# Optimization experiments

Hardware: AMD Instinct MI355X
Metric: run time of the kernel (lower is better)

## Reference

```python
import jax, jax.numpy as jnp
import numpy as np

# Crossbar physical constants (SiOx-like, per crossbar.map conventions)
V_REF = 0.25
K_V = 2.0 * V_REF          # k_V = 2 * V_ref
G_OFF = 1e-4
G_ON = 1e-3
EPS = 1e-12


def setup_inputs() -> dict:
    key = jax.random.key(0)
    ks = jax.random.split(key, 4)
    B, n_in, n_out = 128, 1024, 512
    stdv = 1.0 / np.sqrt(n_in)
    x = jax.random.normal(ks[0], (B, n_in), jnp.float32)
    # non-negative double weights, init N(0.5, stdv) clipped to >=0 (NonNeg constraint)
    w_pos = jnp.maximum(0.5 + stdv * jax.random.normal(ks[1], (n_in, n_out), jnp.float32), 0.0)
    w_neg = jnp.maximum(0.5 + stdv * jax.random.normal(ks[2], (n_in, n_out), jnp.float32), 0.0)
    b_pos = 0.5 * jnp.ones((n_out,), jnp.float32)
    b_neg = 0.5 * jnp.ones((n_out,), jnp.float32)
    # per-device I/V nonlinearity parameter n ~ N(2.132, 0.095), one per crossbar device
    n_param = 2.132 + 0.095 * jax.random.normal(ks[3], (n_in + 1, 2 * n_out), jnp.float32)
    return {"x": x, "w_pos": w_pos, "w_neg": w_neg, "b_pos": b_pos,
            "b_neg": b_neg, "n_param": n_param}


def memristor_dense_fwd(x, w_pos, w_neg, b_pos, b_neg, n_param):
    B = x.shape[0]
    # append ones column for bias row of the crossbar
    inputs = jnp.concatenate([x, jnp.ones((B, 1), x.dtype)], axis=1)      # [B, R], R=n_in+1
    cw_pos = jnp.concatenate([w_pos, b_pos[None, :]], axis=0)             # [R, n_out]
    cw_neg = jnp.concatenate([w_neg, b_neg[None, :]], axis=0)             # [R, n_out]
    # interleave pos/neg columns -> [R, 2*n_out]
    combined = jnp.stack([cw_pos, cw_neg], axis=-1).reshape(cw_pos.shape[0], -1)
    # x -> V  (crossbar.map.x_to_V)
    V = K_V * inputs                                                      # [B, R]
    # w -> G  (crossbar.map.double_w_to_G)
    max_w = jnp.max(combined)
    k_G = (G_ON - G_OFF) / max_w
    G = k_G * combined + G_OFF                                            # [R, C], C=2*n_out
    # IVNonlinearity (LinearityNonpreserving): I = G*V_ref*sign(V)*(|V|/V_ref)^log2(n)
    gamma = jnp.log2(n_param)                                             # [R, C]
    log_ratio = jnp.log(jnp.maximum(jnp.abs(V) / V_REF, EPS))             # [B, R]
    I_ind = (G * V_REF)[None, :, :] * jnp.sign(V)[:, :, None] \
        * jnp.exp(log_ratio[:, :, None] * gamma[None, :, :])              # [B, R, C]
    I = jnp.sum(I_ind, axis=1)                                            # [B, C]
    # I -> y  (crossbar.map.I_to_y): pos - neg columns, undo k_V*k_G scaling
    I_total = I[:, 0::2] - I[:, 1::2]                                     # [B, n_out]
    y = I_total / (K_V * k_G)
    return y


def reference(x, w_pos, w_neg, b_pos, b_neg, n_param):
    return memristor_dense_fwd(x, w_pos, w_neg, b_pos, b_neg, n_param)
```

## Files before the change

kernel.cpp:

```cpp
#include <hip/hip_runtime.h>


#define N_IN 1024
#define N_OUT 512
#define NB 128
#define Z 16
#define RPC 32
#define JT 64
#define BT 16

typedef float v2f __attribute__((ext_vector_type(2)));

#define AOFF 1024
#define BOFF (1024 + Z * NB * N_OUT)

__launch_bounds__(256, 4)
__global__ void memristor_mainAB(const float* __restrict__ x,
                                 const float* __restrict__ wp,
                                 const float* __restrict__ wn,
                                 const float* __restrict__ npar,
                                 float* __restrict__ ws) {
    __shared__ float Wg[RPC][4][16][4];
    __shared__ float Lx[RPC][BT][2];

    const int tid = threadIdx.x;
    const int jx = blockIdx.x, by = blockIdx.y, bz = blockIdx.z;
    const int j0 = jx * JT;
    const int b0 = by * BT;

    const int tj4 = tid & 15;
    const int bl  = tid >> 4;

    v2f accA01 = {0.f, 0.f}, accA23 = {0.f, 0.f};
    v2f accB01 = {0.f, 0.f}, accB23 = {0.f, 0.f};
    float m_w = 0.0f;

    for (int c = 0; c < 2; ++c) {
        const int rbase = bz * 64 + c * RPC;
        __syncthreads();
        {
            int rq = tid & 15;
            float2 v = *(const float2*)&x[(b0 + bl) * N_IN + rbase + rq * 2];
            float vv[2] = {v.x, v.y};
            #pragma unroll
            for (int k = 0; k < 2; ++k) {
                float val = vv[k];
                float s = (val > 0.f) ? 1.f : ((val < 0.f) ? -1.f : 0.f);
                float t = fmaxf(2.f * fabsf(val), 1e-12f);
                Lx[rq * 2 + k][bl][0] = __builtin_amdgcn_logf(t);
                Lx[rq * 2 + k][bl][1] = s;
            }
        }
        {
            int rr = tid >> 3;
            int cg = tid & 7;
            int pg0 = (2 * cg) ^ (rr & 15);
            int pg1 = (2 * cg + 1) ^ (rr & 15);
            {
                const float* prow = &wp[(rbase + rr) * N_OUT + j0 + cg * 8];
                const float* nrow = &wn[(rbase + rr) * N_OUT + j0 + cg * 8];
                float4 pa = *(const float4*)&prow[0];
                float4 pb = *(const float4*)&prow[4];
                float4 na = *(const float4*)&nrow[0];
                float4 nb = *(const float4*)&nrow[4];
                *(float4*)&Wg[rr][0][pg0][0] = pa;
                *(float4*)&Wg[rr][0][pg1][0] = pb;
                *(float4*)&Wg[rr][1][pg0][0] = make_float4(pa.x - na.x, pa.y - na.y,
                                                           pa.z - na.z, pa.w - na.w);
                *(float4*)&Wg[rr][1][pg1][0] = make_float4(pb.x - nb.x, pb.y - nb.y,
                                                           pb.z - nb.z, pb.w - nb.w);
                m_w = fmaxf(m_w, fmaxf(fmaxf(pa.x, pa.y), fmaxf(pa.z, pa.w)));
                m_w = fmaxf(m_w, fmaxf(fmaxf(pb.x, pb.y), fmaxf(pb.z, pb.w)));
                m_w = fmaxf(m_w, fmaxf(fmaxf(na.x, na.y), fmaxf(na.z, na.w)));
                m_w = fmaxf(m_w, fmaxf(fmaxf(nb.x, nb.y), fmaxf(nb.z, nb.w)));
            }
            {
                const float* nrow = &npar[(rbase + rr) * (2 * N_OUT) + 2 * j0 + cg * 16];
                float4 f0 = *(const float4*)&nrow[0];
                float4 f1 = *(const float4*)&nrow[4];
                float4 f2 = *(const float4*)&nrow[8];
                float4 f3 = *(const float4*)&nrow[12];
                *(float4*)&Wg[rr][2][pg0][0] = make_float4(
                    __builtin_amdgcn_logf(f0.x), __builtin_amdgcn_logf(f0.z),
                    __builtin_amdgcn_logf(f1.x), __builtin_amdgcn_logf(f1.z));
                *(float4*)&Wg[rr][3][pg0][0] = make_float4(
                    __builtin_amdgcn_logf(f0.y), __builtin_amdgcn_logf(f0.w),
                    __builtin_amdgcn_logf(f1.y), __builtin_amdgcn_logf(f1.w));
                *(float4*)&Wg[rr][2][pg1][0] = make_float4(
                    __builtin_amdgcn_logf(f2.x), __builtin_amdgcn_logf(f2.z),
                    __builtin_amdgcn_logf(f3.x), __builtin_amdgcn_logf(f3.z));
                *(float4*)&Wg[rr][3][pg1][0] = make_float4(
                    __builtin_amdgcn_logf(f2.y), __builtin_amdgcn_logf(f2.w),
                    __builtin_amdgcn_logf(f3.y), __builtin_amdgcn_logf(f3.w));
            }
        }
        __syncthreads();

        #pragma unroll 4
        for (int r = 0; r < RPC; ++r) {
            const float4* wrow = (const float4*)&Wg[r][0][tj4 ^ (r & 15)][0];
            float4 w_p = wrow[0];
            float4 w_d = wrow[16];
            float4 g_p = wrow[32];
            float4 g_n = wrow[48];
            float2 Ls = *(const float2*)&Lx[r][bl][0];
            const float L = Ls.x, s = Ls.y;

            v2f wp01 = {w_p.x, w_p.y}, wp23 = {w_p.z, w_p.w};
            v2f wd01 = {w_d.x, w_d.y}, wd23 = {w_d.z, w_d.w};
            v2f gp01 = {g_p.x, g_p.y}, gp23 = {g_p.z, g_p.w};
            v2f gn01 = {g_n.x, g_n.y}, gn23 = {g_n.z, g_n.w};

            v2f ap01 = L * gp01, ap23 = L * gp23;
            v2f an01 = L * gn01, an23 = L * gn23;
            v2f ep01, ep23, en01, en23;
            ep01.x = __builtin_amdgcn_exp2f(ap01.x); ep01.y = __builtin_amdgcn_exp2f(ap01.y);
            ep23.x = __builtin_amdgcn_exp2f(ap23.x); ep23.y = __builtin_amdgcn_exp2f(ap23.y);
            en01.x = __builtin_amdgcn_exp2f(an01.x); en01.y = __builtin_amdgcn_exp2f(an01.y);
            en23.x = __builtin_amdgcn_exp2f(an23.x); en23.y = __builtin_amdgcn_exp2f(an23.y);

            v2f u01 = ep01 - en01, u23 = ep23 - en23;
            accB01 += s * u01;
            accB23 += s * u23;
            v2f v01 = wp01 * u01 + wd01 * en01;
            v2f v23 = wp23 * u23 + wd23 * en23;
            accA01 += s * v01;
            accA23 += s * v23;
        }
    }

    {
        size_t base = (size_t)bz * (NB * N_OUT) + (b0 + bl) * N_OUT + j0 + tj4 * 4;
        *(float4*)&ws[AOFF + base] = make_float4(accA01.x, accA01.y, accA23.x, accA23.y);
        *(float4*)&ws[BOFF + base] = make_float4(accB01.x, accB01.y, accB23.x, accB23.y);
    }

    if (by == 0) {
        __syncthreads();
        float* qred = &Lx[0][0][0];
        #pragma unroll
        for (int off = 32; off; off >>= 1) m_w = fmaxf(m_w, __shfl_xor(m_w, off));
        if ((tid & 63) == 0) qred[tid >> 6] = m_w;
        __syncthreads();
        if (tid == 0)
            ws[jx * Z + bz] = fmaxf(fmaxf(qred[0], qred[1]), fmaxf(qred[2], qred[3]));
    }
}

__global__ void reduce_combine(const float* __restrict__ ws,
                               const float* __restrict__ bp,
                               const float* __restrict__ bn,
                               const float* __restrict__ npar,
                               float* __restrict__ out) {
    __shared__ float qs[4];
    const int tid = threadIdx.x;

    float mm = (tid < 128) ? ws[tid] : 0.0f;
    float2 a2 = ((const float2*)bp)[tid];
    float2 b2 = ((const float2*)bn)[tid];
    mm = fmaxf(mm, fmaxf(fmaxf(a2.x, a2.y), fmaxf(b2.x, b2.y)));
    #pragma unroll
    for (int off = 32; off; off >>= 1) mm = fmaxf(mm, __shfl_xor(mm, off));
    if ((tid & 63) == 0) qs[tid >> 6] = mm;
    __syncthreads();
    const float q = fmaxf(fmaxf(qs[0], qs[1]), fmaxf(qs[2], qs[3])) * (1.0f / 9.0f);

    const int g = blockIdx.x * 256 + tid;
    const float4* A4 = (const float4*)(ws + AOFF);
    const float4* B4 = (const float4*)(ws + BOFF);
    float ax = 0.f, ay = 0.f, az = 0.f, aw = 0.f;
    float bx = 0.f, byy = 0.f, bz2 = 0.f, bw = 0.f;
    #pragma unroll
    for (int z = 0; z < Z; ++z) {
        float4 va = A4[(size_t)z * (NB * N_OUT / 4) + g];
        float4 vb = B4[(size_t)z * (NB * N_OUT / 4) + g];
        ax += va.x; ay += va.y; az += va.z; aw += va.w;
        bx += vb.x; byy += vb.y; bz2 += vb.z; bw += vb.w;
    }
    const int j = (g * 4) & (N_OUT - 1);
    float4 bpv = *(const float4*)&bp[j];
    float4 bnv = *(const float4*)&bn[j];
    const float* nrow = &npar[N_IN * (2 * N_OUT) + 2 * j];
    float4 n0 = *(const float4*)&nrow[0];
    float4 n1 = *(const float4*)&nrow[4];
    float y0 = 0.5f * (ax + bpv.x * n0.x - bnv.x * n0.y + q * (bx  + n0.x - n0.y));
    float y1 = 0.5f * (ay + bpv.y * n0.z - bnv.y * n0.w + q * (byy + n0.z - n0.w));
    float y2 = 0.5f * (az + bpv.z * n1.x - bnv.z * n1.y + q * (bz2 + n1.x - n1.y));
    float y3 = 0.5f * (aw + bpv.w * n1.z - bnv.w * n1.w + q * (bw  + n1.z - n1.w));
    ((float4*)out)[g] = make_float4(y0, y1, y2, y3);
}

extern "C" void kernel_launch(void* const* d_in, const int* in_sizes, int n_in,
                              void* d_out, int out_size, void* d_ws, size_t ws_size,
                              hipStream_t stream) {
    const float* x    = (const float*)d_in[0];
    const float* wp   = (const float*)d_in[1];
    const float* wn   = (const float*)d_in[2];
    const float* bp   = (const float*)d_in[3];
    const float* bn   = (const float*)d_in[4];
    const float* npar = (const float*)d_in[5];
    float* out = (float*)d_out;
    float* ws  = (float*)d_ws;

    dim3 grid(N_OUT / JT, NB / BT, Z);
    memristor_mainAB<<<grid, 256, 0, stream>>>(x, wp, wn, npar, ws);

    reduce_combine<<<(NB * N_OUT / 4) / 256, 256, 0, stream>>>(ws, bp, bn, npar, out);
}
```

Baseline: 34.19 us.

## Shrink per-thread tile to two columns and halve batch and row chunks

Each block now covers 8 batch rows instead of 16, and each thread computes 2 output columns instead of 4. Rows are staged in chunks of 16 instead of 32, so there are four chunks, and the launch-bounds occupancy hint rises from 4 to 8. The aim is a larger grid with less work and fewer registers per thread, which gives more waves to hide latency in this exp/log-bound kernel. In exchange, global loads of the weights and log(n) are repeated across twice as many batch blocks, and block-level synchronisation is more frequent.

```diff
diff --git a/kernel.cpp b/kernel.cpp
--- a/kernel.cpp
+++ b/kernel.cpp
@@ -5,16 +5,16 @@
 #define N_OUT 512
 #define NB 128
 #define Z 16
-#define RPC 32
+#define RPC 16
 #define JT 64
-#define BT 16
+#define BT 8
 
 typedef float v2f __attribute__((ext_vector_type(2)));
 
 #define AOFF 1024
 #define BOFF (1024 + Z * NB * N_OUT)
 
-__launch_bounds__(256, 4)
+__launch_bounds__(256, 8)
 __global__ void memristor_mainAB(const float* __restrict__ x,
                                  const float* __restrict__ wp,
                                  const float* __restrict__ wn,
@@ -28,111 +28,83 @@
     const int j0 = jx * JT;
     const int b0 = by * BT;
 
-    const int tj4 = tid & 15;
-    const int bl  = tid >> 4;
+    const int tj2 = tid & 31;
+    const int bl  = tid >> 5;
+    const int g4  = tj2 >> 1;
+    const int sub = (tj2 & 1) * 2;
 
-    v2f accA01 = {0.f, 0.f}, accA23 = {0.f, 0.f};
-    v2f accB01 = {0.f, 0.f}, accB23 = {0.f, 0.f};
+    v2f accA = {0.f, 0.f};
+    v2f accB = {0.f, 0.f};
     float m_w = 0.0f;
 
-    for (int c = 0; c < 2; ++c) {
+    for (int c = 0; c < 4; ++c) {
         const int rbase = bz * 64 + c * RPC;
         __syncthreads();
-        {
+        if (tid < 128) {
+            int bl8 = tid >> 4;
             int rq = tid & 15;
-            float2 v = *(const float2*)&x[(b0 + bl) * N_IN + rbase + rq * 2];
-            float vv[2] = {v.x, v.y};
-            #pragma unroll
-            for (int k = 0; k < 2; ++k) {
-                float val = vv[k];
-                float s = (val > 0.f) ? 1.f : ((val < 0.f) ? -1.f : 0.f);
-                float t = fmaxf(2.f * fabsf(val), 1e-12f);
-                Lx[rq * 2 + k][bl][0] = __builtin_amdgcn_logf(t);
-                Lx[rq * 2 + k][bl][1] = s;
-            }
+            float val = x[(b0 + bl8) * N_IN + rbase + rq];
+            float s = (val > 0.f) ? 1.f : ((val < 0.f) ? -1.f : 0.f);
+            float t = fmaxf(2.f * fabsf(val), 1e-12f);
+            Lx[rq][bl8][0] = __builtin_amdgcn_logf(t);
+            Lx[rq][bl8][1] = s;
         }
         {
-            int rr = tid >> 3;
-            int cg = tid & 7;
-            int pg0 = (2 * cg) ^ (rr & 15);
-            int pg1 = (2 * cg + 1) ^ (rr & 15);
+            int rr = tid >> 4;
+            int cgp = tid & 15;
+            int pg = cgp ^ rr;
             {
-                const float* prow = &wp[(rbase + rr) * N_OUT + j0 + cg * 8];
-                const float* nrow = &wn[(rbase + rr) * N_OUT + j0 + cg * 8];
+                const float* prow = &wp[(rbase + rr) * N_OUT + j0 + cgp * 4];
+                const float* nrow = &wn[(rbase + rr) * N_OUT + j0 + cgp * 4];
                 float4 pa = *(const float4*)&prow[0];
-                float4 pb = *(const float4*)&prow[4];
                 float4 na = *(const float4*)&nrow[0];
-                float4 nb = *(const float4*)&nrow[4];
-                *(float4*)&Wg[rr][0][pg0][0] = pa;
-                *(float4*)&Wg[rr][0][pg1][0] = pb;
-                *(float4*)&Wg[rr][1][pg0][0] = make_float4(pa.x - na.x, pa.y - na.y,
-                                                           pa.z - na.z, pa.w - na.w);
-                *(float4*)&Wg[rr][1][pg1][0] = make_float4(pb.x - nb.x, pb.y - nb.y,
-                                                           pb.z - nb.z, pb.w - nb.w);
+                *(float4*)&Wg[rr][0][pg][0] = pa;
+                *(float4*)&Wg[rr][1][pg][0] = make_float4(pa.x - na.x, pa.y - na.y,
+                                                          pa.z - na.z, pa.w - na.w);
                 m_w = fmaxf(m_w, fmaxf(fmaxf(pa.x, pa.y), fmaxf(pa.z, pa.w)));
-                m_w = fmaxf(m_w, fmaxf(fmaxf(pb.x, pb.y), fmaxf(pb.z, pb.w)));
                 m_w = fmaxf(m_w, fmaxf(fmaxf(na.x, na.y), fmaxf(na.z, na.w)));
-                m_w = fmaxf(m_w, fmaxf(fmaxf(nb.x, nb.y), fmaxf(nb.z, nb.w)));
             }
             {
-                const float* nrow = &npar[(rbase + rr) * (2 * N_OUT) + 2 * j0 + cg * 16];
+                const float* nrow = &npar[(rbase + rr) * (2 * N_OUT) + 2 * j0 + cgp * 8];
                 float4 f0 = *(const float4*)&nrow[0];
                 float4 f1 = *(const float4*)&nrow[4];
-                float4 f2 = *(const float4*)&nrow[8];
-                float4 f3 = *(const float4*)&nrow[12];
-                *(float4*)&Wg[rr][2][pg0][0] = make_float4(
+                *(float4*)&Wg[rr][2][pg][0] = make_float4(
                     __builtin_amdgcn_logf(f0.x), __builtin_amdgcn_logf(f0.z),
                     __builtin_amdgcn_logf(f1.x), __builtin_amdgcn_logf(f1.z));
-                *(float4*)&Wg[rr][3][pg0][0] = make_float4(
+                *(float4*)&Wg[rr][3][pg][0] = make_float4(
                     __builtin_amdgcn_logf(f0.y), __builtin_amdgcn_logf(f0.w),
                     __builtin_amdgcn_logf(f1.y), __builtin_amdgcn_logf(f1.w));
-                *(float4*)&Wg[rr][2][pg1][0] = make_float4(
-                    __builtin_amdgcn_logf(f2.x), __builtin_amdgcn_logf(f2.z),
-                    __builtin_amdgcn_logf(f3.x), __builtin_amdgcn_logf(f3.z));
-                *(float4*)&Wg[rr][3][pg1][0] = make_float4(
-                    __builtin_amdgcn_logf(f2.y), __builtin_amdgcn_logf(f2.w),
-                    __builtin_amdgcn_logf(f3.y), __builtin_amdgcn_logf(f3.w));
             }
         }
         __syncthreads();
 
-        #pragma unroll 4
+        #pragma unroll 8
         for (int r = 0; r < RPC; ++r) {
-            const float4* wrow = (const float4*)&Wg[r][0][tj4 ^ (r & 15)][0];
-            float4 w_p = wrow[0];
-            float4 w_d = wrow[16];
-            float4 g_p = wrow[32];
-            float4 g_n = wrow[48];
+            const float* wbase = &Wg[r][0][g4 ^ r][sub];
+            v2f w_p = *(const v2f*)&wbase[0];
+            v2f w_d = *(const v2f*)&wbase[64];
+            v2f g_p = *(const v2f*)&wbase[128];
+            v2f g_n = *(const v2f*)&wbase[192];
             float2 Ls = *(const float2*)&Lx[r][bl][0];
             const float L = Ls.x, s = Ls.y;
 
-            v2f wp01 = {w_p.x, w_p.y}, wp23 = {w_p.z, w_p.w};
-            v2f wd01 = {w_d.x, w_d.y}, wd23 = {w_d.z, w_d.w};
-            v2f gp01 = {g_p.x, g_p.y}, gp23 = {g_p.z, g_p.w};
-            v2f gn01 = {g_n.x, g_n.y}, gn23 = {g_n.z, g_n.w};
+            v2f ap = L * g_p;
+            v2f an = L * g_n;
+            v2f ep, en;
+            ep.x = __builtin_amdgcn_exp2f(ap.x); ep.y = __builtin_amdgcn_exp2f(ap.y);
+            en.x = __builtin_amdgcn_exp2f(an.x); en.y = __builtin_amdgcn_exp2f(an.y);
 
-            v2f ap01 = L * gp01, ap23 = L * gp23;
-            v2f an01 = L * gn01, an23 = L * gn23;
-            v2f ep01, ep23, en01, en23;
-            ep01.x = __builtin_amdgcn_exp2f(ap01.x); ep01.y = __builtin_amdgcn_exp2f(ap01.y);
-            ep23.x = __builtin_amdgcn_exp2f(ap23.x); ep23.y = __builtin_amdgcn_exp2f(ap23.y);
-            en01.x = __builtin_amdgcn_exp2f(an01.x); en01.y = __builtin_amdgcn_exp2f(an01.y);
-            en23.x = __builtin_amdgcn_exp2f(an23.x); en23.y = __builtin_amdgcn_exp2f(an23.y);
-
-            v2f u01 = ep01 - en01, u23 = ep23 - en23;
-            accB01 += s * u01;
-            accB23 += s * u23;
-            v2f v01 = wp01 * u01 + wd01 * en01;
-            v2f v23 = wp23 * u23 + wd23 * en23;
-            accA01 += s * v01;
-            accA23 += s * v23;
+            v2f u = ep - en;
+            accB += s * u;
+            v2f v = w_p * u + w_d * en;
+            accA += s * v;
         }
     }
 
     {
-        size_t base = (size_t)bz * (NB * N_OUT) + (b0 + bl) * N_OUT + j0 + tj4 * 4;
-        *(float4*)&ws[AOFF + base] = make_float4(accA01.x, accA01.y, accA23.x, accA23.y);
-        *(float4*)&ws[BOFF + base] = make_float4(accB01.x, accB01.y, accB23.x, accB23.y);
+        size_t base = (size_t)bz * (NB * N_OUT) + (b0 + bl) * N_OUT + j0 + tj2 * 2;
+        *(float2*)&ws[AOFF + base] = make_float2(accA.x, accA.y);
+        *(float2*)&ws[BOFF + base] = make_float2(accB.x, accB.y);
     }
 
     if (by == 0) {
```

Measured after the change: 37.56 us. 1.1x slower.

## Fuse split-K reduction into main kernel via atomic counter grid barrier

Applied to the files above, without the earlier changes.

Merges the separate reduce_combine launch into the main kernel. Every block increments a global atomic counter, and the blocks with the last z-index spin until all 1024 blocks have arrived, then reduce the 16 partial slabs and write the output. A hipMemsetAsync clears the counter before each launch, and the inner loop unroll goes from 4 to 8. This removes one kernel launch and its gap, but it relies on all blocks being co-resident or scheduled in an order that avoids deadlock, and the spinning blocks hold CU slots while they wait.

```diff
diff --git a/kernel.cpp b/kernel.cpp
--- a/kernel.cpp
+++ b/kernel.cpp
@@ -15,11 +15,14 @@
 #define BOFF (1024 + Z * NB * N_OUT)
 
 __launch_bounds__(256, 4)
-__global__ void memristor_mainAB(const float* __restrict__ x,
-                                 const float* __restrict__ wp,
-                                 const float* __restrict__ wn,
-                                 const float* __restrict__ npar,
-                                 float* __restrict__ ws) {
+__global__ void memristor_one(const float* __restrict__ x,
+                              const float* __restrict__ wp,
+                              const float* __restrict__ wn,
+                              const float* __restrict__ bp,
+                              const float* __restrict__ bn,
+                              const float* __restrict__ npar,
+                              float* __restrict__ ws,
+                              float* __restrict__ out) {
     __shared__ float Wg[RPC][4][16][4];
     __shared__ float Lx[RPC][BT][2];
 
@@ -27,6 +30,8 @@
     const int jx = blockIdx.x, by = blockIdx.y, bz = blockIdx.z;
     const int j0 = jx * JT;
     const int b0 = by * BT;
+    unsigned* acnt = (unsigned*)ws;
+    float* slots = ws + 16;
 
     const int tj4 = tid & 15;
     const int bl  = tid >> 4;
@@ -75,11 +80,11 @@
                 m_w = fmaxf(m_w, fmaxf(fmaxf(nb.x, nb.y), fmaxf(nb.z, nb.w)));
             }
             {
-                const float* nrow = &npar[(rbase + rr) * (2 * N_OUT) + 2 * j0 + cg * 16];
-                float4 f0 = *(const float4*)&nrow[0];
-                float4 f1 = *(const float4*)&nrow[4];
-                float4 f2 = *(const float4*)&nrow[8];
-                float4 f3 = *(const float4*)&nrow[12];
+                const float* grow = &npar[(rbase + rr) * (2 * N_OUT) + 2 * j0 + cg * 16];
+                float4 f0 = *(const float4*)&grow[0];
+                float4 f1 = *(const float4*)&grow[4];
+                float4 f2 = *(const float4*)&grow[8];
+                float4 f3 = *(const float4*)&grow[12];
                 *(float4*)&Wg[rr][2][pg0][0] = make_float4(
                     __builtin_amdgcn_logf(f0.x), __builtin_amdgcn_logf(f0.z),
                     __builtin_amdgcn_logf(f1.x), __builtin_amdgcn_logf(f1.z));
@@ -96,7 +101,7 @@
         }
         __syncthreads();
 
-        #pragma unroll 4
+        #pragma unroll 8
         for (int r = 0; r < RPC; ++r) {
             const float4* wrow = (const float4*)&Wg[r][0][tj4 ^ (r & 15)][0];
             float4 w_p = wrow[0];
@@ -135,59 +140,71 @@
         *(float4*)&ws[BOFF + base] = make_float4(accB01.x, accB01.y, accB23.x, accB23.y);
     }
 
+    __syncthreads();
     if (by == 0) {
-        __syncthreads();
         float* qred = &Lx[0][0][0];
         #pragma unroll
         for (int off = 32; off; off >>= 1) m_w = fmaxf(m_w, __shfl_xor(m_w, off));
         if ((tid & 63) == 0) qred[tid >> 6] = m_w;
         __syncthreads();
         if (tid == 0)
-            ws[jx * Z + bz] = fmaxf(fmaxf(qred[0], qred[1]), fmaxf(qred[2], qred[3]));
-    }
-}
-
-__global__ void reduce_combine(const float* __restrict__ ws,
-                               const float* __restrict__ bp,
-                               const float* __restrict__ bn,
-                               const float* __restrict__ npar,
-                               float* __restrict__ out) {
-    __shared__ float qs[4];
-    const int tid = threadIdx.x;
-
-    float mm = (tid < 128) ? ws[tid] : 0.0f;
-    float2 a2 = ((const float2*)bp)[tid];
-    float2 b2 = ((const float2*)bn)[tid];
-    mm = fmaxf(mm, fmaxf(fmaxf(a2.x, a2.y), fmaxf(b2.x, b2.y)));
-    #pragma unroll
-    for (int off = 32; off; off >>= 1) mm = fmaxf(mm, __shfl_xor(mm, off));
-    if ((tid & 63) == 0) qs[tid >> 6] = mm;
+            slots[jx * Z + bz] = fmaxf(fmaxf(qred[0], qred[1]), fmaxf(qred[2], qred[3]));
+    }
+
+    if (tid == 0) {
+        __threadfence();
+        __hip_atomic_fetch_add(acnt, 1u, __ATOMIC_RELEASE, __HIP_MEMORY_SCOPE_AGENT);
+    }
+
+    if (bz != Z - 1) return;
+
+    if (tid == 0) {
+        while (__hip_atomic_load(acnt, __ATOMIC_RELAXED, __HIP_MEMORY_SCOPE_AGENT) < 1024u)
+            __builtin_amdgcn_s_sleep(2);
+    }
     __syncthreads();
-    const float q = fmaxf(fmaxf(qs[0], qs[1]), fmaxf(qs[2], qs[3])) * (1.0f / 9.0f);
-
-    const int g = blockIdx.x * 256 + tid;
-    const float4* A4 = (const float4*)(ws + AOFF);
-    const float4* B4 = (const float4*)(ws + BOFF);
-    float ax = 0.f, ay = 0.f, az = 0.f, aw = 0.f;
-    float bx = 0.f, byy = 0.f, bz2 = 0.f, bw = 0.f;
-    #pragma unroll
-    for (int z = 0; z < Z; ++z) {
-        float4 va = A4[(size_t)z * (NB * N_OUT / 4) + g];
-        float4 vb = B4[(size_t)z * (NB * N_OUT / 4) + g];
-        ax += va.x; ay += va.y; az += va.z; aw += va.w;
-        bx += vb.x; byy += vb.y; bz2 += vb.z; bw += vb.w;
-    }
-    const int j = (g * 4) & (N_OUT - 1);
-    float4 bpv = *(const float4*)&bp[j];
-    float4 bnv = *(const float4*)&bn[j];
-    const float* nrow = &npar[N_IN * (2 * N_OUT) + 2 * j];
-    float4 n0 = *(const float4*)&nrow[0];
-    float4 n1 = *(const float4*)&nrow[4];
-    float y0 = 0.5f * (ax + bpv.x * n0.x - bnv.x * n0.y + q * (bx  + n0.x - n0.y));
-    float y1 = 0.5f * (ay + bpv.y * n0.z - bnv.y * n0.w + q * (byy + n0.z - n0.w));
-    float y2 = 0.5f * (az + bpv.z * n1.x - bnv.z * n1.y + q * (bz2 + n1.x - n1.y));
-    float y3 = 0.5f * (aw + bpv.w * n1.z - bnv.w * n1.w + q * (bw  + n1.z - n1.w));
-    ((float4*)out)[g] = make_float4(y0, y1, y2, y3);
+    __builtin_amdgcn_fence(__ATOMIC_ACQUIRE, "agent");
+
+    float q;
+    {
+        float mm = (tid < 128) ? slots[tid] : 0.0f;
+        float2 a2 = ((const float2*)bp)[tid];
+        float2 b2 = ((const float2*)bn)[tid];
+        mm = fmaxf(mm, fmaxf(fmaxf(a2.x, a2.y), fmaxf(b2.x, b2.y)));
+        #pragma unroll
+        for (int off = 32; off; off >>= 1) mm = fmaxf(mm, __shfl_xor(mm, off));
+        float* qs = &Lx[0][0][0];
+        __syncthreads();
+        if ((tid & 63) == 0) qs[tid >> 6] = mm;
+        __syncthreads();
+        q = fmaxf(fmaxf(qs[0], qs[1]), fmaxf(qs[2], qs[3])) * (1.0f / 9.0f);
+    }
+
+    {
+        int bb = tid >> 4, j4 = tid & 15;
+        const float* colA = ws + AOFF + (b0 + bb) * N_OUT + j0 + j4 * 4;
+        const float* colB = ws + BOFF + (b0 + bb) * N_OUT + j0 + j4 * 4;
+        float ax = 0.f, ay = 0.f, az = 0.f, aw = 0.f;
+        float bx = 0.f, byv = 0.f, bzv = 0.f, bw = 0.f;
+        #pragma unroll
+        for (int z = 0; z < Z; ++z) {
+            float4 va = *(const float4*)(colA + (size_t)z * (NB * N_OUT));
+            float4 vb = *(const float4*)(colB + (size_t)z * (NB * N_OUT));
+            ax += va.x; ay += va.y; az += va.z; aw += va.w;
+            bx += vb.x; byv += vb.y; bzv += vb.z; bw += vb.w;
+        }
+        int j = j0 + j4 * 4;
+        float4 bpv = *(const float4*)&bp[j];
+        float4 bnv = *(const float4*)&bn[j];
+        const float* nrow = &npar[N_IN * (2 * N_OUT) + 2 * j];
+        float4 n0 = *(const float4*)&nrow[0];
+        float4 n1 = *(const float4*)&nrow[4];
+        float y0 = 0.5f * (ax + bpv.x * n0.x - bnv.x * n0.y + q * (bx  + n0.x - n0.y));
+        float y1 = 0.5f * (ay + bpv.y * n0.z - bnv.y * n0.w + q * (byv + n0.z - n0.w));
+        float y2 = 0.5f * (az + bpv.z * n1.x - bnv.z * n1.y + q * (bzv + n1.x - n1.y));
+        float y3 = 0.5f * (aw + bpv.w * n1.z - bnv.w * n1.w + q * (bw  + n1.z - n1.w));
+        *(float4*)&out[(b0 + bb) * N_OUT + j] = make_float4(y0, y1, y2, y3);
+    }
 }
 
 extern "C" void kernel_launch(void* const* d_in, const int* in_sizes, int n_in,
@@ -202,8 +219,8 @@
     float* out = (float*)d_out;
     float* ws  = (float*)d_ws;
 
+    hipMemsetAsync(d_ws, 0, 8, stream);
+
     dim3 grid(N_OUT / JT, NB / BT, Z);
-    memristor_mainAB<<<grid, 256, 0, stream>>>(x, wp, wn, npar, ws);
-
-    reduce_combine<<<(NB * N_OUT / 4) / 256, 256, 0, stream>>>(ws, bp, bn, npar, out);
+    memristor_one<<<grid, 256, 0, stream>>>(x, wp, wn, bp, bn, npar, ws, out);
 }
```

After: 79.16 us. +131.5%, slower.

## Enlarge batch tile to reuse staged weights and store partials in fp16

Applied to the files above, without the earlier changes.

Each thread now computes four batch rows per column group (BT 16→64), so the weight and log-parameter tiles staged in shared memory are loaded once and reused across more batch rows. This cuts grid size by 4x and the redundant npar log work. Split-K partial sums are written as fp16 instead of fp32, halving the workspace traffic. The reduce kernel is reshaped to 64-thread blocks with a single-wave max reduction. The fp16 partials risk accuracy loss, and the larger tile raises register pressure and lowers occupancy.

```diff
diff --git a/kernel.cpp b/kernel.cpp
--- a/kernel.cpp
+++ b/kernel.cpp
@@ -7,14 +7,14 @@
 #define Z 16
 #define RPC 32
 #define JT 64
-#define BT 16
+#define BT 64
 
 typedef float v2f __attribute__((ext_vector_type(2)));
-
-#define AOFF 1024
-#define BOFF (1024 + Z * NB * N_OUT)
-
-__launch_bounds__(256, 4)
+typedef _Float16 h4 __attribute__((ext_vector_type(4)));
+
+#define PLEN (Z * NB * N_OUT)
+
+__launch_bounds__(256, 2)
 __global__ void memristor_mainAB(const float* __restrict__ x,
                                  const float* __restrict__ wp,
                                  const float* __restrict__ wn,
@@ -29,26 +29,33 @@
     const int b0 = by * BT;
 
     const int tj4 = tid & 15;
-    const int bl  = tid >> 4;
-
-    v2f accA01 = {0.f, 0.f}, accA23 = {0.f, 0.f};
-    v2f accB01 = {0.f, 0.f}, accB23 = {0.f, 0.f};
+    const int bl0 = (tid >> 4) * 4;
+
+    v2f accA[4][2];
+    v2f accB[4][2];
+    #pragma unroll
+    for (int i = 0; i < 4; ++i) {
+        accA[i][0] = (v2f){0.f, 0.f}; accA[i][1] = (v2f){0.f, 0.f};
+        accB[i][0] = (v2f){0.f, 0.f}; accB[i][1] = (v2f){0.f, 0.f};
+    }
     float m_w = 0.0f;
 
     for (int c = 0; c < 2; ++c) {
         const int rbase = bz * 64 + c * RPC;
         __syncthreads();
         {
-            int rq = tid & 15;
-            float2 v = *(const float2*)&x[(b0 + bl) * N_IN + rbase + rq * 2];
-            float vv[2] = {v.x, v.y};
+            int bl = tid & 63;
+            int rq = tid >> 6;
+            float4 v0 = *(const float4*)&x[(b0 + bl) * N_IN + rbase + rq * 8];
+            float4 v1 = *(const float4*)&x[(b0 + bl) * N_IN + rbase + rq * 8 + 4];
+            float vv[8] = {v0.x, v0.y, v0.z, v0.w, v1.x, v1.y, v1.z, v1.w};
             #pragma unroll
-            for (int k = 0; k < 2; ++k) {
+            for (int k = 0; k < 8; ++k) {
                 float val = vv[k];
                 float s = (val > 0.f) ? 1.f : ((val < 0.f) ? -1.f : 0.f);
                 float t = fmaxf(2.f * fabsf(val), 1e-12f);
-                Lx[rq * 2 + k][bl][0] = __builtin_amdgcn_logf(t);
-                Lx[rq * 2 + k][bl][1] = s;
+                Lx[rq * 8 + k][bl][0] = __builtin_amdgcn_logf(t);
+                Lx[rq * 8 + k][bl][1] = s;
             }
         }
         {
@@ -75,11 +82,11 @@
                 m_w = fmaxf(m_w, fmaxf(fmaxf(nb.x, nb.y), fmaxf(nb.z, nb.w)));
             }
             {
-                const float* nrow = &npar[(rbase + rr) * (2 * N_OUT) + 2 * j0 + cg * 16];
-                float4 f0 = *(const float4*)&nrow[0];
-                float4 f1 = *(const float4*)&nrow[4];
-                float4 f2 = *(const float4*)&nrow[8];
-                float4 f3 = *(const float4*)&nrow[12];
+                const float* grow = &npar[(rbase + rr) * (2 * N_OUT) + 2 * j0 + cg * 16];
+                float4 f0 = *(const float4*)&grow[0];
+                float4 f1 = *(const float4*)&grow[4];
+                float4 f2 = *(const float4*)&grow[8];
+                float4 f3 = *(const float4*)&grow[12];
                 *(float4*)&Wg[rr][2][pg0][0] = make_float4(
                     __builtin_amdgcn_logf(f0.x), __builtin_amdgcn_logf(f0.z),
                     __builtin_amdgcn_logf(f1.x), __builtin_amdgcn_logf(f1.z));
@@ -103,36 +110,50 @@
             float4 w_d = wrow[16];
             float4 g_p = wrow[32];
             float4 g_n = wrow[48];
-            float2 Ls = *(const float2*)&Lx[r][bl][0];
-            const float L = Ls.x, s = Ls.y;
+            float4 l01 = *(const float4*)&Lx[r][bl0][0];
+            float4 l23 = *(const float4*)&Lx[r][bl0 + 2][0];
 
             v2f wp01 = {w_p.x, w_p.y}, wp23 = {w_p.z, w_p.w};
             v2f wd01 = {w_d.x, w_d.y}, wd23 = {w_d.z, w_d.w};
             v2f gp01 = {g_p.x, g_p.y}, gp23 = {g_p.z, g_p.w};
             v2f gn01 = {g_n.x, g_n.y}, gn23 = {g_n.z, g_n.w};
-
-            v2f ap01 = L * gp01, ap23 = L * gp23;
-            v2f an01 = L * gn01, an23 = L * gn23;
-            v2f ep01, ep23, en01, en23;
-            ep01.x = __builtin_amdgcn_exp2f(ap01.x); ep01.y = __builtin_amdgcn_exp2f(ap01.y);
-            ep23.x = __builtin_amdgcn_exp2f(ap23.x); ep23.y = __builtin_amdgcn_exp2f(ap23.y);
-            en01.x = __builtin_amdgcn_exp2f(an01.x); en01.y = __builtin_amdgcn_exp2f(an01.y);
-            en23.x = __builtin_amdgcn_exp2f(an23.x); en23.y = __builtin_amdgcn_exp2f(an23.y);
-
-            v2f u01 = ep01 - en01, u23 = ep23 - en23;
-            accB01 += s * u01;
-            accB23 += s * u23;
-            v2f v01 = wp01 * u01 + wd01 * en01;
-            v2f v23 = wp23 * u23 + wd23 * en23;
-            accA01 += s * v01;
-            accA23 += s * v23;
+            float Lv[4] = {l01.x, l01.z, l23.x, l23.z};
+            float Sv[4] = {l01.y, l01.w, l23.y, l23.w};
+
+            #pragma unroll
+            for (int ib = 0; ib < 4; ++ib) {
+                const float L = Lv[ib], s = Sv[ib];
+                v2f ap01 = L * gp01, ap23 = L * gp23;
+                v2f an01 = L * gn01, an23 = L * gn23;
+                v2f ep01, ep23, en01, en23;
+                ep01.x = __builtin_amdgcn_exp2f(ap01.x); ep01.y = __builtin_amdgcn_exp2f(ap01.y);
+                ep23.x = __builtin_amdgcn_exp2f(ap23.x); ep23.y = __builtin_amdgcn_exp2f(ap23.y);
+                en01.x = __builtin_amdgcn_exp2f(an01.x); en01.y = __builtin_amdgcn_exp2f(an01.y);
+                en23.x = __builtin_amdgcn_exp2f(an23.x); en23.y = __builtin_amdgcn_exp2f(an23.y);
+                v2f u01 = ep01 - en01, u23 = ep23 - en23;
+                accB[ib][0] += s * u01;
+                accB[ib][1] += s * u23;
+                v2f v01 = wp01 * u01 + wd01 * en01;
+                v2f v23 = wp23 * u23 + wd23 * en23;
+                accA[ib][0] += s * v01;
+                accA[ib][1] += s * v23;
+            }
         }
     }
 
     {
-        size_t base = (size_t)bz * (NB * N_OUT) + (b0 + bl) * N_OUT + j0 + tj4 * 4;
-        *(float4*)&ws[AOFF + base] = make_float4(accA01.x, accA01.y, accA23.x, accA23.y);
-        *(float4*)&ws[BOFF + base] = make_float4(accB01.x, accB01.y, accB23.x, accB23.y);
+        _Float16* hA = (_Float16*)(ws + 1024);
+        _Float16* hB = hA + PLEN;
+        size_t base = (size_t)bz * (NB * N_OUT) + (b0 + bl0) * N_OUT + j0 + tj4 * 4;
+        #pragma unroll
+        for (int ib = 0; ib < 4; ++ib) {
+            h4 ha = {(_Float16)accA[ib][0].x, (_Float16)accA[ib][0].y,
+                     (_Float16)accA[ib][1].x, (_Float16)accA[ib][1].y};
+            h4 hb = {(_Float16)accB[ib][0].x, (_Float16)accB[ib][0].y,
+                     (_Float16)accB[ib][1].x, (_Float16)accB[ib][1].y};
+            *(h4*)&hA[base + (size_t)ib * N_OUT] = ha;
+            *(h4*)&hB[base + (size_t)ib * N_OUT] = hb;
+        }
     }
 
     if (by == 0) {
@@ -152,30 +173,33 @@
                                const float* __restrict__ bn,
                                const float* __restrict__ npar,
                                float* __restrict__ out) {
-    __shared__ float qs[4];
     const int tid = threadIdx.x;
-
-    float mm = (tid < 128) ? ws[tid] : 0.0f;
-    float2 a2 = ((const float2*)bp)[tid];
-    float2 b2 = ((const float2*)bn)[tid];
-    mm = fmaxf(mm, fmaxf(fmaxf(a2.x, a2.y), fmaxf(b2.x, b2.y)));
+    const int g = blockIdx.x * 64 + tid;
+
+    float mm = fmaxf(ws[tid], ws[tid + 64]);
+    {
+        const float4* b4 = (const float4*)&bp[tid * 8];
+        const float4* c4 = (const float4*)&bn[tid * 8];
+        float4 p0 = b4[0], p1 = b4[1], q0 = c4[0], q1 = c4[1];
+        mm = fmaxf(mm, fmaxf(fmaxf(p0.x, p0.y), fmaxf(p0.z, p0.w)));
+        mm = fmaxf(mm, fmaxf(fmaxf(p1.x, p1.y), fmaxf(p1.z, p1.w)));
+        mm = fmaxf(mm, fmaxf(fmaxf(q0.x, q0.y), fmaxf(q0.z, q0.w)));
+        mm = fmaxf(mm, fmaxf(fmaxf(q1.x, q1.y), fmaxf(q1.z, q1.w)));
+    }
     #pragma unroll
     for (int off = 32; off; off >>= 1) mm = fmaxf(mm, __shfl_xor(mm, off));
-    if ((tid & 63) == 0) qs[tid >> 6] = mm;
-    __syncthreads();
-    const float q = fmaxf(fmaxf(qs[0], qs[1]), fmaxf(qs[2], qs[3])) * (1.0f / 9.0f);
-
-    const int g = blockIdx.x * 256 + tid;
-    const float4* A4 = (const float4*)(ws + AOFF);
-    const float4* B4 = (const float4*)(ws + BOFF);
+    const float q = mm * (1.0f / 9.0f);
+
+    const h4* hA = (const h4*)((const _Float16*)(ws + 1024));
+    const h4* hB = hA + PLEN / 4;
     float ax = 0.f, ay = 0.f, az = 0.f, aw = 0.f;
     float bx = 0.f, byy = 0.f, bz2 = 0.f, bw = 0.f;
     #pragma unroll
     for (int z = 0; z < Z; ++z) {
-        float4 va = A4[(size_t)z * (NB * N_OUT / 4) + g];
-        float4 vb = B4[(size_t)z * (NB * N_OUT / 4) + g];
-        ax += va.x; ay += va.y; az += va.z; aw += va.w;
-        bx += vb.x; byy += vb.y; bz2 += vb.z; bw += vb.w;
+        h4 va = hA[(size_t)z * (NB * N_OUT / 4) + g];
+        h4 vb = hB[(size_t)z * (NB * N_OUT / 4) + g];
+        ax += (float)va.x; ay += (float)va.y; az += (float)va.z; aw += (float)va.w;
+        bx += (float)vb.x; byy += (float)vb.y; bz2 += (float)vb.z; bw += (float)vb.w;
     }
     const int j = (g * 4) & (N_OUT - 1);
     float4 bpv = *(const float4*)&bp[j];
@@ -205,5 +229,5 @@
     dim3 grid(N_OUT / JT, NB / BT, Z);
     memristor_mainAB<<<grid, 256, 0, stream>>>(x, wp, wn, npar, ws);
 
-    reduce_combine<<<(NB * N_OUT / 4) / 256, 256, 0, stream>>>(ws, bp, bn, npar, out);
+    reduce_combine<<<(NB * N_OUT / 4) / 64, 64, 0, stream>>>(ws, bp, bn, npar, out);
 }
```

New measurement: 30.27 us. 1.13x faster.
